# Kernel tuning notes

Measured on AMD Instinct MI355X. Metric: run time of the kernel, lower is better.

## Reference

```python
import jax, jax.numpy as jnp
import numpy as np

B = 256              # board_size
F = B - 1            # node feature dim
N = B                # number of nodes (forced by flatten -> l4)
E = 65536            # directed edges
H = 2048             # hidden_layer_size
OUT = B * (B - 1) // 2


def _edge_conv(x, src, dst, W1, b1, W2, b2, W3, b3):
    # PyG EdgeConv: max_j nn([x_i, x_j - x_i]); edge_index = [source j, target i]
    xi = x[dst]                                   # [E, F]
    xj = x[src]                                   # [E, F]
    h = jnp.concatenate([xi, xj - xi], axis=-1)   # [E, 2F]
    h = h @ W1.T + b1                             # [E, 2F]
    h = h @ W2.T + b2                             # [E, F]
    h = h @ W3.T + b3                             # [E, F]
    agg = jax.ops.segment_max(h, dst, num_segments=x.shape[0])
    # empty segments come back as -inf -> 0 (PyG fill behavior)
    return jnp.where(jnp.isfinite(agg), agg, 0.0)


def _lin_init(k, o, i):
    kw, kb = jax.random.split(k)
    lim = 1.0 / np.sqrt(i)
    W = jax.random.uniform(kw, (o, i), jnp.float32, -lim, lim)
    b = jax.random.uniform(kb, (o,), jnp.float32, -lim, lim)
    return W, b


def setup_inputs() -> dict:
    key = jax.random.key(0)
    ks = jax.random.split(key, 16)
    d = {}
    d["x"] = jax.random.normal(ks[0], (N, F), jnp.float32)
    d["edge_index"] = jax.random.randint(ks[1], (2, E), 0, N)
    idx = 2
    for l in ("ec1", "ec2", "ec3"):
        for nm, o, i in (("1", 2 * F, 2 * F), ("2", F, 2 * F), ("3", F, F)):
            W, b = _lin_init(ks[idx], o, i); idx += 1
            d[f"{l}_W{nm}"] = W
            d[f"{l}_b{nm}"] = b
    d["l4_W"], d["l4_b"] = _lin_init(ks[idx], H, N * F); idx += 1
    d["out_W"], d["out_b"] = _lin_init(ks[idx], OUT, H)
    return d


def reference(x, edge_index,
              ec1_W1, ec1_b1, ec1_W2, ec1_b2, ec1_W3, ec1_b3,
              ec2_W1, ec2_b1, ec2_W2, ec2_b2, ec2_W3, ec2_b3,
              ec3_W1, ec3_b1, ec3_W2, ec3_b2, ec3_W3, ec3_b3,
              l4_W, l4_b, out_W, out_b):
    src, dst = edge_index[0], edge_index[1]
    g1 = jax.nn.relu(_edge_conv(x, src, dst, ec1_W1, ec1_b1, ec1_W2, ec1_b2, ec1_W3, ec1_b3))
    g2 = jax.nn.relu(_edge_conv(g1, src, dst, ec2_W1, ec2_b1, ec2_W2, ec2_b2, ec2_W3, ec2_b3) + g1)
    g3 = jax.nn.relu(_edge_conv(g2, src, dst, ec3_W1, ec3_b1, ec3_W2, ec3_b2, ec3_W3, ec3_b3) + g2)
    y = jax.nn.relu(l4_W @ g3.ravel() + l4_b)     # mat-vec, [H]
    return out_W @ y + out_b                      # [OUT]
```

## Files before the change

### kernel.cpp

```cpp
#include <hip/hip_runtime.h>
#include <math.h>

#define NNODE 256
#define FF    255
#define F2    510
#define EE    65536
#define HH    2048
#define OUTN  32640

typedef float vf4 __attribute__((ext_vector_type(4)));

#define OFF_W1P 0
#define OFF_W2P 786432
#define OFF_W3P 1179648
#define OFF_T   1376256
#define OFF_K   1769472
#define OFF_KDT 2162688
#define OFF_KBT 2359296
#define OFF_BEFF 2555904
#define OFF_GP  2556672
#define OFF_U   2818816
#define OFF_V   2884352
#define OFF_G3C 2949888
#define OFF_Y   3015168
#define OFF_MASK_BYTES (3017216L*4)

struct PrepArgs {
    const float* x;
    const int*   ei;
    const float* W1[3]; const float* b1[3];
    const float* W2[3]; const float* b2[3];
    const float* W3[3]; const float* b3[3];
};

__global__ __launch_bounds__(256) void prep_kernel(PrepArgs a, float* __restrict__ ws,
                                                   unsigned long long* __restrict__ mask) {
    int b = blockIdx.x, t = threadIdx.x;
    if (b < 1536) {
        int l = b >> 9, r = b & 511;
        const float* W1 = a.W1[l]; const float* b1 = a.b1[l];
        float* dst = ws + OFF_W1P + l * (512 * 512) + r * 512;
        for (int c = t; c < 512; c += 256) {
            float v = 0.f;
            if (r < F2 && c < F2)      v = W1[r * F2 + c];
            else if (c == F2)          v = (r < F2) ? b1[r] : ((r == F2) ? 1.f : 0.f);
            dst[c] = v;
        }
    } else if (b < 2304) {
        int bb = b - 1536; int l = bb >> 8, r = bb & 255;
        const float* W2 = a.W2[l]; const float* b2 = a.b2[l];
        float* dst = ws + OFF_W2P + l * (256 * 512) + r * 512;
        for (int c = t; c < 512; c += 256) {
            float v = 0.f;
            if (r < FF && c < F2)      v = W2[r * F2 + c];
            else if (c == F2)          v = (r < FF) ? b2[r] : 1.f;
            dst[c] = v;
        }
    } else if (b < 3072) {
        int bb = b - 2304; int l = bb >> 8, r = bb & 255;
        float* dst = ws + OFF_W3P + l * (256 * 256) + r * 256;
        float v = 0.f;
        if (r < FF) {
            if (t < FF)       v = a.W3[l][r * FF + t];
            else if (t == FF) v = a.b3[l][r];
        }
        dst[t] = v;
    } else if (b < 3328) {
        int r = b - 3072;
        float* dst = ws + OFF_GP + r * 256;
        dst[t] = (t < FF) ? a.x[r * FF + t] : 0.f;
    } else {
        int e = (b - 3328) * 256 + t;
        int s = a.ei[e];
        int d = a.ei[EE + e];
        atomicOr(&mask[d * 4 + (s >> 6)], 1ull << (s & 63));
    }
}

template <int KDIM, int NCOL>
__global__ __launch_bounds__(256) void rowgemm(const float* __restrict__ A, long sA,
                                               const float* __restrict__ B, long sB,
                                               float* __restrict__ C, long sC) {
    A += (long)blockIdx.z * sA + (long)blockIdx.x * 4 * KDIM;
    B += (long)blockIdx.z * sB;
    C += (long)blockIdx.z * sC + (long)blockIdx.x * 4 * NCOL;
    int t = threadIdx.x;
    if (NCOL == 512) {
        const float2* B2 = (const float2*)B;
        float2 a0 = {0.f, 0.f}, a1 = {0.f, 0.f}, a2 = {0.f, 0.f}, a3 = {0.f, 0.f};
        #pragma unroll 4
        for (int k = 0; k < KDIM; k++) {
            float2 bv = B2[k * (NCOL / 2) + t];
            float w0 = A[0 * KDIM + k], w1 = A[1 * KDIM + k];
            float w2 = A[2 * KDIM + k], w3 = A[3 * KDIM + k];
            a0.x += w0 * bv.x; a0.y += w0 * bv.y;
            a1.x += w1 * bv.x; a1.y += w1 * bv.y;
            a2.x += w2 * bv.x; a2.y += w2 * bv.y;
            a3.x += w3 * bv.x; a3.y += w3 * bv.y;
        }
        float2* C2 = (float2*)C;
        C2[0 * (NCOL / 2) + t] = a0;
        C2[1 * (NCOL / 2) + t] = a1;
        C2[2 * (NCOL / 2) + t] = a2;
        C2[3 * (NCOL / 2) + t] = a3;
    } else {
        float a0 = 0.f, a1 = 0.f, a2 = 0.f, a3 = 0.f;
        #pragma unroll 4
        for (int k = 0; k < KDIM; k++) {
            float bv = B[k * NCOL + t];
            a0 += A[0 * KDIM + k] * bv;
            a1 += A[1 * KDIM + k] * bv;
            a2 += A[2 * KDIM + k] * bv;
            a3 += A[3 * KDIM + k] * bv;
        }
        C[0 * NCOL + t] = a0;
        C[1 * NCOL + t] = a1;
        C[2 * NCOL + t] = a2;
        C[3 * NCOL + t] = a3;
    }
}

__global__ __launch_bounds__(256) void split_kernel(float* __restrict__ ws) {
    int l = blockIdx.y, k = blockIdx.x, o = threadIdx.x;
    const float* Kp = ws + OFF_K + l * 131072;
    if (k < 256) {
        float d = 0.f, bb = 0.f;
        if (k < FF) {
            float k1 = Kp[o * 512 + k];
            float k2 = Kp[o * 512 + FF + k];
            d = k1 - k2; bb = k2;
        }
        ws[OFF_KDT + l * 65536 + k * 256 + o] = d;
        ws[OFF_KBT + l * 65536 + k * 256 + o] = bb;
    } else {
        ws[OFF_BEFF + l * 256 + o] = Kp[o * 512 + F2];
    }
}

__global__ __launch_bounds__(256) void agg_kernel(const float* __restrict__ U,
                                                  const float* __restrict__ V,
                                                  const float* __restrict__ beff,
                                                  const float* __restrict__ gprev,
                                                  float* __restrict__ gout,
                                                  float* __restrict__ g3c,
                                                  const unsigned long long* __restrict__ mask,
                                                  int has_res) {
    int i = blockIdx.x, f = threadIdx.x;
    __shared__ unsigned long long mw[4];
    if (f < 4) mw[f] = mask[i * 4 + f];
    __syncthreads();
    unsigned long long m0 = mw[0], m1 = mw[1], m2 = mw[2], m3 = mw[3];
    unsigned long long mr[4] = {m0, m1, m2, m3};
    float vm = -INFINITY;
    #pragma unroll
    for (int w = 0; w < 4; w++) {
        unsigned long long mword = mr[w];
        const float* Vp = V + w * 64 * 256 + f;
        #pragma unroll 8
        for (int j = 0; j < 64; j++) {
            float v = Vp[j * 256];
            vm = ((mword >> j) & 1) ? fmaxf(vm, v) : vm;
        }
    }
    bool any = (m0 | m1 | m2 | m3) != 0ull;
    float val = any ? (U[i * 256 + f] + beff[f] + vm) : 0.f;
    if (has_res) val += gprev[i * 256 + f];
    float g = fmaxf(val, 0.f);
    gout[i * 256 + f] = g;
    if (g3c && f < FF) g3c[i * FF + f] = g;
}

__global__ __launch_bounds__(256) void l4_kernel(const float* __restrict__ W,
                                                 const float* __restrict__ bias,
                                                 const float* __restrict__ g3c,
                                                 float* __restrict__ y) {
    int row0 = blockIdx.x * 2;
    int t = threadIdx.x;
    const vf4* W4 = (const vf4*)W;
    const vf4* G4 = (const vf4*)g3c;
    const int K4 = 65280 / 4;
    float a0 = 0.f, a1 = 0.f;
    const vf4* w0p = W4 + (long)(row0 + 0) * K4;
    const vf4* w1p = W4 + (long)(row0 + 1) * K4;
    for (int v = t; v < K4; v += 256) {
        vf4 g  = G4[v];
        vf4 w0 = __builtin_nontemporal_load(&w0p[v]);
        vf4 w1 = __builtin_nontemporal_load(&w1p[v]);
        a0 += w0.x * g.x + w0.y * g.y + w0.z * g.z + w0.w * g.w;
        a1 += w1.x * g.x + w1.y * g.y + w1.z * g.z + w1.w * g.w;
    }
    #pragma unroll
    for (int off = 32; off; off >>= 1) {
        a0 += __shfl_xor(a0, off);
        a1 += __shfl_xor(a1, off);
    }
    __shared__ float red[4][2];
    int wv = t >> 6, ln = t & 63;
    if (ln == 0) { red[wv][0] = a0; red[wv][1] = a1; }
    __syncthreads();
    if (t < 2) {
        float s = red[0][t] + red[1][t] + red[2][t] + red[3][t];
        y[row0 + t] = fmaxf(s + bias[row0 + t], 0.f);
    }
}

__global__ __launch_bounds__(256) void out_kernel(const float* __restrict__ W,
                                                  const float* __restrict__ bias,
                                                  const float* __restrict__ y,
                                                  float* __restrict__ out) {
    int wv = threadIdx.x >> 6, ln = threadIdx.x & 63;
    int r = blockIdx.x * 4 + wv;
    const vf4* W4 = (const vf4*)(W + (long)r * HH);
    const vf4* Y4 = (const vf4*)y;
    float acc = 0.f;
    #pragma unroll
    for (int i = 0; i < 8; i++) {
        vf4 w  = __builtin_nontemporal_load(&W4[ln + 64 * i]);
        vf4 yy = Y4[ln + 64 * i];
        acc += w.x * yy.x + w.y * yy.y + w.z * yy.z + w.w * yy.w;
    }
    #pragma unroll
    for (int off = 32; off; off >>= 1) acc += __shfl_xor(acc, off);
    if (ln == 0) out[r] = acc + bias[r];
}

extern "C" void kernel_launch(void* const* d_in, const int* in_sizes, int n_in,
                              void* d_out, int out_size, void* d_ws, size_t ws_size,
                              hipStream_t stream) {
    float* ws = (float*)d_ws;
    unsigned long long* mask = (unsigned long long*)((char*)d_ws + OFF_MASK_BYTES);

    PrepArgs pa;
    pa.x  = (const float*)d_in[0];
    pa.ei = (const int*)d_in[1];
    for (int l = 0; l < 3; l++) {
        pa.W1[l] = (const float*)d_in[2 + l * 6 + 0];
        pa.b1[l] = (const float*)d_in[2 + l * 6 + 1];
        pa.W2[l] = (const float*)d_in[2 + l * 6 + 2];
        pa.b2[l] = (const float*)d_in[2 + l * 6 + 3];
        pa.W3[l] = (const float*)d_in[2 + l * 6 + 4];
        pa.b3[l] = (const float*)d_in[2 + l * 6 + 5];
    }
    const float* l4W  = (const float*)d_in[20];
    const float* l4b  = (const float*)d_in[21];
    const float* outW = (const float*)d_in[22];
    const float* outb = (const float*)d_in[23];

    (void)hipMemsetAsync(mask, 0, 8192, stream);
    prep_kernel<<<3584, 256, 0, stream>>>(pa, ws, mask);

    rowgemm<512, 512><<<dim3(64, 1, 3), 256, 0, stream>>>(
        ws + OFF_W2P, 131072, ws + OFF_W1P, 262144, ws + OFF_T, 131072);
    rowgemm<256, 512><<<dim3(64, 1, 3), 256, 0, stream>>>(
        ws + OFF_W3P, 65536, ws + OFF_T, 131072, ws + OFF_K, 131072);
    split_kernel<<<dim3(257, 3), 256, 0, stream>>>(ws);

    for (int l = 0; l < 3; l++) {
        const float* gprev = ws + OFF_GP + l * 65536;
        float* gout = ws + OFF_GP + (l + 1) * 65536;
        rowgemm<256, 256><<<dim3(64, 1, 2), 256, 0, stream>>>(
            gprev, 0, ws + OFF_KDT + l * 65536, OFF_KBT - OFF_KDT, ws + OFF_U, 65536);
        agg_kernel<<<256, 256, 0, stream>>>(
            ws + OFF_U, ws + OFF_V, ws + OFF_BEFF + l * 256,
            gprev, gout, (l == 2) ? (ws + OFF_G3C) : nullptr, mask, (l > 0) ? 1 : 0);
    }

    l4_kernel<<<1024, 256, 0, stream>>>(l4W, l4b, ws + OFF_G3C, ws + OFF_Y);
    out_kernel<<<8160, 256, 0, stream>>>(outW, outb, ws + OFF_Y, (float*)d_out);
}
```

Baseline: 1.045 ms.

## Fuse K-split into weight GEMM and fuse aggregation with next-layer GEMM

Folds the separate split/transposition kernel into the W3·T product so KdT/KbT/beff are written directly from shared memory. It also fuses each layer's masked max aggregation with the next layer's U/V projection, which cuts the launch count and avoids round-trips of g through global memory. l4 now uses one row per block instead of two. The fused kernels run on only 64 blocks, so parallelism drops. The U2/V2 buffers now alias the old K region, which is safe because K is no longer materialized.

```diff
diff --git a/kernel.cpp b/kernel.cpp
--- a/kernel.cpp
+++ b/kernel.cpp
@@ -15,6 +15,8 @@
 #define OFF_W3P 1179648
 #define OFF_T   1376256
 #define OFF_K   1769472
+#define OFF_U2  OFF_K
+#define OFF_V2  (OFF_K + 65536)
 #define OFF_KDT 2162688
 #define OFF_KBT 2359296
 #define OFF_BEFF 2555904
@@ -120,21 +122,101 @@
     }
 }
 
-__global__ __launch_bounds__(256) void split_kernel(float* __restrict__ ws) {
-    int l = blockIdx.y, k = blockIdx.x, o = threadIdx.x;
-    const float* Kp = ws + OFF_K + l * 131072;
-    if (k < 256) {
-        float d = 0.f, bb = 0.f;
-        if (k < FF) {
-            float k1 = Kp[o * 512 + k];
-            float k2 = Kp[o * 512 + FF + k];
-            d = k1 - k2; bb = k2;
-        }
-        ws[OFF_KDT + l * 65536 + k * 256 + o] = d;
-        ws[OFF_KBT + l * 65536 + k * 256 + o] = bb;
-    } else {
-        ws[OFF_BEFF + l * 256 + o] = Kp[o * 512 + F2];
-    }
+__global__ __launch_bounds__(256) void rowgemmK(float* __restrict__ ws) {
+    int l = blockIdx.z, t = threadIdx.x, r0 = blockIdx.x * 4;
+    const float*  A  = ws + OFF_W3P + l * 65536 + r0 * 256;
+    const float2* B2 = (const float2*)(ws + OFF_T + l * 131072);
+    float2 a0 = {0.f, 0.f}, a1 = {0.f, 0.f}, a2 = {0.f, 0.f}, a3 = {0.f, 0.f};
+    #pragma unroll 4
+    for (int k = 0; k < 256; k++) {
+        float2 bv = B2[k * 256 + t];
+        float w0 = A[0 * 256 + k], w1 = A[1 * 256 + k];
+        float w2 = A[2 * 256 + k], w3 = A[3 * 256 + k];
+        a0.x += w0 * bv.x; a0.y += w0 * bv.y;
+        a1.x += w1 * bv.x; a1.y += w1 * bv.y;
+        a2.x += w2 * bv.x; a2.y += w2 * bv.y;
+        a3.x += w3 * bv.x; a3.y += w3 * bv.y;
+    }
+    __shared__ float Kt[4][512];
+    Kt[0][2 * t] = a0.x; Kt[0][2 * t + 1] = a0.y;
+    Kt[1][2 * t] = a1.x; Kt[1][2 * t + 1] = a1.y;
+    Kt[2][2 * t] = a2.x; Kt[2][2 * t + 1] = a2.y;
+    Kt[3][2 * t] = a3.x; Kt[3][2 * t + 1] = a3.y;
+    __syncthreads();
+    float* KdT = ws + OFF_KDT + l * 65536;
+    float* KbT = ws + OFF_KBT + l * 65536;
+    if (t < FF) {
+        #pragma unroll
+        for (int r = 0; r < 4; r++) {
+            float k1 = Kt[r][t], k2 = Kt[r][FF + t];
+            KdT[t * 256 + r0 + r] = k1 - k2;
+            KbT[t * 256 + r0 + r] = k2;
+        }
+    } else if (t == FF) {
+        #pragma unroll
+        for (int r = 0; r < 4; r++) {
+            KdT[FF * 256 + r0 + r] = 0.f;
+            KbT[FF * 256 + r0 + r] = 0.f;
+        }
+    }
+    if (t < 4) ws[OFF_BEFF + l * 256 + r0 + t] = Kt[t][F2];
+}
+
+template <int HAS_RES>
+__global__ __launch_bounds__(256) void agg_gemm(const float* __restrict__ U,
+                                                const float* __restrict__ V,
+                                                const float* __restrict__ beff,
+                                                const float* __restrict__ gprev,
+                                                float* __restrict__ gout,
+                                                const unsigned long long* __restrict__ mask,
+                                                const float* __restrict__ Bd,
+                                                const float* __restrict__ Bb,
+                                                float* __restrict__ Uo,
+                                                float* __restrict__ Vo) {
+    int r0 = blockIdx.x * 4, t = threadIdx.x;
+    __shared__ float gs[4][256];
+    __shared__ unsigned long long ms[4][4];
+    if (t < 16) ms[t >> 2][t & 3] = mask[r0 * 4 + t];
+    __syncthreads();
+    float vm0 = -INFINITY, vm1 = -INFINITY, vm2 = -INFINITY, vm3 = -INFINITY;
+    #pragma unroll
+    for (int w = 0; w < 4; w++) {
+        unsigned long long w0 = ms[0][w], w1 = ms[1][w], w2 = ms[2][w], w3 = ms[3][w];
+        const float* Vp = V + w * 64 * 256 + t;
+        #pragma unroll 8
+        for (int j = 0; j < 64; j++) {
+            float v = Vp[j * 256];
+            vm0 = ((w0 >> j) & 1) ? fmaxf(vm0, v) : vm0;
+            vm1 = ((w1 >> j) & 1) ? fmaxf(vm1, v) : vm1;
+            vm2 = ((w2 >> j) & 1) ? fmaxf(vm2, v) : vm2;
+            vm3 = ((w3 >> j) & 1) ? fmaxf(vm3, v) : vm3;
+        }
+    }
+    float be = beff[t];
+    float vms[4] = {vm0, vm1, vm2, vm3};
+    #pragma unroll
+    for (int i = 0; i < 4; i++) {
+        bool any = (ms[i][0] | ms[i][1] | ms[i][2] | ms[i][3]) != 0ull;
+        float val = any ? (U[(r0 + i) * 256 + t] + be + vms[i]) : 0.f;
+        if (HAS_RES) val += gprev[(r0 + i) * 256 + t];
+        float g = fmaxf(val, 0.f);
+        gs[i][t] = g;
+        gout[(r0 + i) * 256 + t] = g;
+    }
+    __syncthreads();
+    float u0 = 0.f, u1 = 0.f, u2 = 0.f, u3 = 0.f;
+    float v0 = 0.f, v1 = 0.f, v2 = 0.f, v3 = 0.f;
+    #pragma unroll 4
+    for (int k = 0; k < 256; k++) {
+        float bd = Bd[k * 256 + t], bb = Bb[k * 256 + t];
+        float g0 = gs[0][k], g1 = gs[1][k], g2 = gs[2][k], g3 = gs[3][k];
+        u0 += g0 * bd; u1 += g1 * bd; u2 += g2 * bd; u3 += g3 * bd;
+        v0 += g0 * bb; v1 += g1 * bb; v2 += g2 * bb; v3 += g3 * bb;
+    }
+    Uo[(r0 + 0) * 256 + t] = u0; Uo[(r0 + 1) * 256 + t] = u1;
+    Uo[(r0 + 2) * 256 + t] = u2; Uo[(r0 + 3) * 256 + t] = u3;
+    Vo[(r0 + 0) * 256 + t] = v0; Vo[(r0 + 1) * 256 + t] = v1;
+    Vo[(r0 + 2) * 256 + t] = v2; Vo[(r0 + 3) * 256 + t] = v3;
 }
 
 __global__ __launch_bounds__(256) void agg_kernel(const float* __restrict__ U,
@@ -174,34 +256,23 @@
                                                  const float* __restrict__ bias,
                                                  const float* __restrict__ g3c,
                                                  float* __restrict__ y) {
-    int row0 = blockIdx.x * 2;
-    int t = threadIdx.x;
-    const vf4* W4 = (const vf4*)W;
+    int row = blockIdx.x, t = threadIdx.x;
+    const int K4 = 65280 / 4;
+    const vf4* Wp = (const vf4*)W + (long)row * K4;
     const vf4* G4 = (const vf4*)g3c;
-    const int K4 = 65280 / 4;
-    float a0 = 0.f, a1 = 0.f;
-    const vf4* w0p = W4 + (long)(row0 + 0) * K4;
-    const vf4* w1p = W4 + (long)(row0 + 1) * K4;
+    float a = 0.f;
     for (int v = t; v < K4; v += 256) {
-        vf4 g  = G4[v];
-        vf4 w0 = __builtin_nontemporal_load(&w0p[v]);
-        vf4 w1 = __builtin_nontemporal_load(&w1p[v]);
-        a0 += w0.x * g.x + w0.y * g.y + w0.z * g.z + w0.w * g.w;
-        a1 += w1.x * g.x + w1.y * g.y + w1.z * g.z + w1.w * g.w;
-    }
-    #pragma unroll
-    for (int off = 32; off; off >>= 1) {
-        a0 += __shfl_xor(a0, off);
-        a1 += __shfl_xor(a1, off);
-    }
-    __shared__ float red[4][2];
+        vf4 g = G4[v];
+        vf4 w = __builtin_nontemporal_load(&Wp[v]);
+        a += w.x * g.x + w.y * g.y + w.z * g.z + w.w * g.w;
+    }
+    #pragma unroll
+    for (int off = 32; off; off >>= 1) a += __shfl_xor(a, off);
+    __shared__ float red[4];
     int wv = t >> 6, ln = t & 63;
-    if (ln == 0) { red[wv][0] = a0; red[wv][1] = a1; }
-    __syncthreads();
-    if (t < 2) {
-        float s = red[0][t] + red[1][t] + red[2][t] + red[3][t];
-        y[row0 + t] = fmaxf(s + bias[row0 + t], 0.f);
-    }
+    if (ln == 0) red[wv] = a;
+    __syncthreads();
+    if (t == 0) y[row] = fmaxf(red[0] + red[1] + red[2] + red[3] + bias[row], 0.f);
 }
 
 __global__ __launch_bounds__(256) void out_kernel(const float* __restrict__ W,
@@ -251,20 +322,22 @@
 
     rowgemm<512, 512><<<dim3(64, 1, 3), 256, 0, stream>>>(
         ws + OFF_W2P, 131072, ws + OFF_W1P, 262144, ws + OFF_T, 131072);
-    rowgemm<256, 512><<<dim3(64, 1, 3), 256, 0, stream>>>(
-        ws + OFF_W3P, 65536, ws + OFF_T, 131072, ws + OFF_K, 131072);
-    split_kernel<<<dim3(257, 3), 256, 0, stream>>>(ws);
-
-    for (int l = 0; l < 3; l++) {
-        const float* gprev = ws + OFF_GP + l * 65536;
-        float* gout = ws + OFF_GP + (l + 1) * 65536;
-        rowgemm<256, 256><<<dim3(64, 1, 2), 256, 0, stream>>>(
-            gprev, 0, ws + OFF_KDT + l * 65536, OFF_KBT - OFF_KDT, ws + OFF_U, 65536);
-        agg_kernel<<<256, 256, 0, stream>>>(
-            ws + OFF_U, ws + OFF_V, ws + OFF_BEFF + l * 256,
-            gprev, gout, (l == 2) ? (ws + OFF_G3C) : nullptr, mask, (l > 0) ? 1 : 0);
-    }
-
-    l4_kernel<<<1024, 256, 0, stream>>>(l4W, l4b, ws + OFF_G3C, ws + OFF_Y);
+    rowgemmK<<<dim3(64, 1, 3), 256, 0, stream>>>(ws);
+
+    rowgemm<256, 256><<<dim3(64, 1, 2), 256, 0, stream>>>(
+        ws + OFF_GP, 0, ws + OFF_KDT, OFF_KBT - OFF_KDT, ws + OFF_U, 65536);
+
+    agg_gemm<0><<<64, 256, 0, stream>>>(
+        ws + OFF_U, ws + OFF_V, ws + OFF_BEFF, ws + OFF_GP, ws + OFF_GP + 65536, mask,
+        ws + OFF_KDT + 65536, ws + OFF_KBT + 65536, ws + OFF_U2, ws + OFF_V2);
+    agg_gemm<1><<<64, 256, 0, stream>>>(
+        ws + OFF_U2, ws + OFF_V2, ws + OFF_BEFF + 256, ws + OFF_GP + 65536,
+        ws + OFF_GP + 2 * 65536, mask,
+        ws + OFF_KDT + 2 * 65536, ws + OFF_KBT + 2 * 65536, ws + OFF_U, ws + OFF_V);
+    agg_kernel<<<256, 256, 0, stream>>>(
+        ws + OFF_U, ws + OFF_V, ws + OFF_BEFF + 512, ws + OFF_GP + 2 * 65536,
+        ws + OFF_GP + 3 * 65536, ws + OFF_G3C, mask, 1);
+
+    l4_kernel<<<2048, 256, 0, stream>>>(l4W, l4b, ws + OFF_G3C, ws + OFF_Y);
     out_kernel<<<8160, 256, 0, stream>>>(outW, outb, ws + OFF_Y, (float*)d_out);
 }
```

New measurement: 1.046 ms. No clear change (+0.1%).
